# Kernel optimization log

Measured on AMD Instinct MI355X. Metric: run time of the kernel, lower is better.

Reference implementation:

```python
import jax, jax.numpy as jnp
import numpy as np

SPATIAL_DIM = 2
N_IN = 4096
N_OUT = 1024
C_IN = 32
C_OUT = 32
FILTER_SEQ = (64, 64)
BATCH = 16


def _grid(num_points):
    # replicates: meshgrid(indexing='xy') of linspace(0,1,n) per dim, dstack, view(-1, d)
    n = int(num_points ** (1.0 / SPATIAL_DIM))
    nodes = np.linspace(0.0, 1.0, n)
    X, Y = np.meshgrid(nodes, nodes, indexing='xy')
    return np.dstack((X, Y)).reshape(-1, SPATIAL_DIM)  # (n^2, 2)


def _cache():
    # replicates QuadConvLayer.cache(): bump-support sparsity pattern
    out_locs = _grid(N_OUT)               # (N_OUT, 2)
    in_nodes = _grid(N_IN)                # (N_IN, 2)
    locs = out_locs[:, None, :] - in_nodes[None, :, :]   # (N_OUT, N_IN, 2)
    bump_arg = np.linalg.norm(locs, axis=2) ** 4
    decay_param = (N_IN / 16.0) ** 2
    mask = bump_arg <= 1.0 / decay_param
    idx = np.argwhere(mask)               # (E, 2), row-major sorted like torch.nonzero
    eval_locs = locs[mask]                # (E, 2)
    return eval_locs.astype(np.float32), idx.astype(np.int64)


def setup_inputs() -> dict:
    key = jax.random.key(0)
    k_feat, k1, k2, k3 = jax.random.split(key, 4)
    eval_locs, eval_indices = _cache()
    # filter MLP G: Linear(2,64,bias=False) -> Sin -> Linear(64,64) -> Sin -> Linear(64, C_IN*C_OUT)
    d0, d1, d2, d3 = SPATIAL_DIM, FILTER_SEQ[0], FILTER_SEQ[1], C_IN * C_OUT
    W1 = jax.random.normal(k1, (d0, d1), jnp.float32) / np.sqrt(d0)
    W2 = jax.random.normal(k2, (d1, d2), jnp.float32) / np.sqrt(d1)
    W3 = jax.random.normal(k3, (d2, d3), jnp.float32) / np.sqrt(d2)
    features = jax.random.normal(k_feat, (BATCH, C_IN, N_IN), jnp.float32)
    return {
        "features": features,
        "W1": W1,
        "W2": W2,
        "W3": W3,
        "eval_locs": jnp.asarray(eval_locs),
        "eval_indices": jnp.asarray(eval_indices),
    }


def reference(features, W1, W2, W3, eval_locs, eval_indices):
    B = features.shape[0]
    E = eval_locs.shape[0]
    seg = eval_indices[:, 0]   # output point per edge (sorted)
    src = eval_indices[:, 1]   # input point per edge
    # filter MLP with Sin activations: (E, 2) -> (E, C_IN, C_OUT)
    h = jnp.sin(eval_locs @ W1)
    h = jnp.sin(h @ W2)
    filt = (h @ W3).reshape(E, C_IN, C_OUT)
    # gather features at source points: (B, C_IN, E)
    gathered = features[:, :, src]
    # faithful to torch: a raw reshape (NOT a transpose) of (B, C_IN, E) -> (B, E, C_IN)
    g = gathered.reshape(B, E, C_IN)
    vals = jnp.einsum('bni,nij->bnj', g, filt)   # (B, E, C_OUT)
    # faithful raw reshape (B, E, C_OUT) -> (B, C_OUT, E)
    vals = vals.reshape(B, C_OUT, E)
    # scatter-sum over edges into output points (segment_coo sum)
    integral = jnp.zeros((B, C_OUT, N_OUT), features.dtype).at[:, :, seg].add(vals)
    return integral
```

## Files before the change

kernel.cpp:

```cpp
#include <hip/hip_runtime.h>
#include <hip/hip_bf16.h>

typedef __bf16 bf16x4  __attribute__((ext_vector_type(4)));
typedef __bf16 bf16x8  __attribute__((ext_vector_type(8)));
typedef __bf16 bf16x16 __attribute__((ext_vector_type(16)));
typedef float  f32x4   __attribute__((ext_vector_type(4)));

#define N_IN   4096
#define N_OUT  1024
#define BATCH  16
#define ROWS   16

#define H1_STR   72
#define H2_STR   72
#define FT_JSTR  40
#define FTH_NSTR 648
#define G_STR    520
#define V_STR    520
#define GSTR2    1048
#define VSTR2    1288
#define FB_FT_NSTR 1288
#define SEG_STR  34
#define TILE_K   144

#define WS_W3T_OFF    0
#define WS_W2T_OFF    131072
#define WS_FEATT_OFF  139264
#define WS_NEED       4333568

__global__ void qc_zero_kernel(float* __restrict__ out, int n4) {
    int i = blockIdx.x * blockDim.x + threadIdx.x;
    if (i < n4) ((float4*)out)[i] = make_float4(0.f, 0.f, 0.f, 0.f);
}

__global__ void qc_prep_kernel(const float* __restrict__ w3, const float* __restrict__ w2,
                               __bf16* __restrict__ w3t, __bf16* __restrict__ w2t) {
    int gid = blockIdx.x * blockDim.x + threadIdx.x;
    if (gid < 65536) {
        int k = gid & 63, col = gid >> 6;
        w3t[gid] = (__bf16)w3[k * 1024 + col];
    } else {
        int j = gid - 65536;
        int k = j & 63, col = j >> 6;
        w2t[j] = (__bf16)w2[k * 64 + col];
    }
}

__global__ void qc_prep2_kernel(const float* __restrict__ w3, const float* __restrict__ w2,
                                const float* __restrict__ feat,
                                float* __restrict__ out,
                                __bf16* __restrict__ w3t, __bf16* __restrict__ w2t,
                                __bf16* __restrict__ featT) {
    int bid = blockIdx.x, tid = threadIdx.x;
    if (bid < 512) {
        int c    = bid >> 4;
        int src  = (bid & 15) * 256 + tid;
        bf16x16 v;
        #pragma unroll
        for (int b = 0; b < 16; ++b)
            v[b] = (__bf16)feat[(b * 32 + c) * N_IN + src];
        __bf16* p = &featT[((size_t)c * N_IN + src) * 16];
        *(bf16x8*)p       = *(bf16x8*)&v;
        *(bf16x8*)(p + 8) = *((bf16x8*)&v + 1);
    } else if (bid < 528) {
        __shared__ float tile[64][65];
        const int colbase = (bid - 512) * 64;
        #pragma unroll
        for (int it = 0; it < 16; ++it) {
            int k = it * 4 + (tid >> 6);
            int c = tid & 63;
            tile[k][c] = w3[k * 1024 + colbase + c];
        }
        __syncthreads();
        int cc = tid >> 2;
        int k0 = (tid & 3) * 16;
        bf16x8 o0, o1;
        #pragma unroll
        for (int z = 0; z < 8; ++z) {
            o0[z] = (__bf16)tile[k0 + z][cc];
            o1[z] = (__bf16)tile[k0 + 8 + z][cc];
        }
        __bf16* wp = &w3t[(colbase + cc) * 64 + k0];
        *(bf16x8*)wp       = o0;
        *(bf16x8*)(wp + 8) = o1;
    } else if (bid == 528) {
        #pragma unroll
        for (int z = 0; z < 16; ++z) {
            int j = tid * 16 + z;
            w2t[j] = (__bf16)w2[(j & 63) * 64 + (j >> 6)];
        }
    } else {
        int i = (bid - 529) * 256 + tid;
        ((float4*)out)[i] = make_float4(0.f, 0.f, 0.f, 0.f);
    }
}

__global__ __launch_bounds__(512, 2)
void qc_fused32_kernel(const __bf16* __restrict__ featT,
                       const float* __restrict__ w1,
                       const float* __restrict__ locs,
                       const int*   __restrict__ eidx,
                       const __bf16* __restrict__ w2t,
                       const __bf16* __restrict__ w3t,
                       float* __restrict__ out,
                       int E)
{
    __shared__ __align__(16) unsigned char region1[41472];
    __shared__ __align__(16) unsigned char region2[9216];
    __shared__ unsigned short seg_s[32 * SEG_STR];

    __bf16* gb   = (__bf16*)region1;
    __bf16* ftv  = (__bf16*)region1;
    __bf16* vals = (__bf16*)region1;

    __bf16* h1b  = (__bf16*)region2;
    __bf16* h2b  = (__bf16*)(region2 + 9216/2);
    float*  tile = (float*)region2;

    const int tid  = threadIdx.x;
    const int lane = tid & 63;
    const int wv   = tid >> 6;
    const int ml   = lane & 15;
    const int q    = lane >> 4;
    const int n0   = blockIdx.x * 32;
    const int t0   = n0 * 32;
    const int ch0  = t0 / E;
    const int m0   = t0 - ch0 * E;

    const int tlb = wv * 128 + lane;
    bf16x16 gvv[2];
    int sgv[2];
    #pragma unroll
    for (int h = 0; h < 2; ++h) {
        int tl = tlb + h * 64;
        int mm = m0 + tl;
        int cc = ch0 + (mm >= E);
        if (mm >= E) mm -= E;
        int2 p = ((const int2*)eidx)[mm];
        sgv[h] = p.x;
        int ccc = cc < 32 ? cc : 31;
        bf16x16 g = *(const bf16x16*)&featT[((size_t)ccc * N_IN + p.y) * 16];
        if (cc >= 32) {
            #pragma unroll
            for (int z = 0; z < 16; ++z) g[z] = (__bf16)0.f;
        }
        gvv[h] = g;
    }
    const int rg = (wv >> 2) * 16;
    const int cw = (wv & 3) * 16;
    const bf16x8 bw0 = *(const bf16x8*)&w2t[(cw + ml) * 64 + q * 8];
    const bf16x8 bw1 = *(const bf16x8*)&w2t[(cw + ml) * 64 + 32 + q * 8];

    {
        const int r  = tid >> 4;
        const int j0 = (tid & 15) * 4;
        float lx = 0.f, ly = 0.f;
        int n = n0 + r;
        if (n < E) { lx = locs[n * 2]; ly = locs[n * 2 + 1]; }
        float4 wa = *(const float4*)&w1[j0];
        float4 wb = *(const float4*)&w1[64 + j0];
        __bf16* hp = &h1b[r * H1_STR + j0];
        hp[0] = (__bf16)__sinf(lx * wa.x + ly * wb.x);
        hp[1] = (__bf16)__sinf(lx * wa.y + ly * wb.y);
        hp[2] = (__bf16)__sinf(lx * wa.z + ly * wb.z);
        hp[3] = (__bf16)__sinf(lx * wa.w + ly * wb.w);
    }
    __syncthreads();

    {
        bf16x8 a0 = *(const bf16x8*)&h1b[(rg + ml) * H1_STR + q * 8];
        bf16x8 a1 = *(const bf16x8*)&h1b[(rg + ml) * H1_STR + 32 + q * 8];
        f32x4 c = {0.f, 0.f, 0.f, 0.f};
        c = __builtin_amdgcn_mfma_f32_16x16x32_bf16(a0, bw0, c, 0, 0, 0);
        c = __builtin_amdgcn_mfma_f32_16x16x32_bf16(a1, bw1, c, 0, 0, 0);
        #pragma unroll
        for (int g_ = 0; g_ < 4; ++g_)
            h2b[(rg + q * 4 + g_) * H2_STR + cw + ml] = (__bf16)__sinf(c[g_]);
    }

    #pragma unroll
    for (int b = 0; b < 16; ++b) {
        gb[b * GSTR2 + tlb]      = gvv[0][b];
        gb[b * GSTR2 + tlb + 64] = gvv[1][b];
    }
    seg_s[(tlb >> 5) * SEG_STR + (tlb & 31)] = (unsigned short)sgv[0];
    {
        int tl1 = tlb + 64;
        seg_s[(tl1 >> 5) * SEG_STR + (tl1 & 31)] = (unsigned short)sgv[1];
    }
    bf16x8 ag[4];
    #pragma unroll
    for (int rr = 0; rr < 4; ++rr)
        ag[rr] = *(const bf16x8*)&gb[ml * GSTR2 + (wv * 4 + rr) * 32 + q * 8];
    __syncthreads();

    bf16x8 ha00 = *(const bf16x8*)&h2b[ml * H2_STR + q * 8];
    bf16x8 ha01 = *(const bf16x8*)&h2b[ml * H2_STR + 32 + q * 8];
    bf16x8 ha10 = *(const bf16x8*)&h2b[(16 + ml) * H2_STR + q * 8];
    bf16x8 ha11 = *(const bf16x8*)&h2b[(16 + ml) * H2_STR + 32 + q * 8];

    f32x4 c0[4], c1[4];

    {
        f32x4 accA[4], accB[4];
        #pragma unroll
        for (int tt = 0; tt < 4; ++tt) {
            int i_  = wv * 4 + tt;
            int col = i_ * 32 + ml;
            const __bf16* wp = &w3t[col * 64 + q * 8];
            bf16x8 b0 = *(const bf16x8*)wp;
            bf16x8 b1 = *(const bf16x8*)(wp + 32);
            f32x4 cA = {0.f, 0.f, 0.f, 0.f};
            f32x4 cB = {0.f, 0.f, 0.f, 0.f};
            cA = __builtin_amdgcn_mfma_f32_16x16x32_bf16(ha00, b0, cA, 0, 0, 0);
            cA = __builtin_amdgcn_mfma_f32_16x16x32_bf16(ha01, b1, cA, 0, 0, 0);
            cB = __builtin_amdgcn_mfma_f32_16x16x32_bf16(ha10, b0, cB, 0, 0, 0);
            cB = __builtin_amdgcn_mfma_f32_16x16x32_bf16(ha11, b1, cB, 0, 0, 0);
            accA[tt] = cA; accB[tt] = cB;
        }
        #pragma unroll
        for (int g_ = 0; g_ < 4; ++g_) {
            bf16x4 pa, pb;
            #pragma unroll
            for (int tt = 0; tt < 4; ++tt) {
                pa[tt] = (__bf16)accA[tt][g_];
                pb[tt] = (__bf16)accB[tt][g_];
            }
            *(bf16x4*)&ftv[(q * 4 + g_) * FTH_NSTR + ml * FT_JSTR + wv * 4]        = pa;
            *(bf16x4*)&ftv[(16 + q * 4 + g_) * FTH_NSTR + ml * FT_JSTR + wv * 4]   = pb;
        }
    }
    __syncthreads();

    #pragma unroll
    for (int z = 0; z < 5; ++z) {
        int i = tid + z * 512;
        if (i < 16 * TILE_K) tile[i] = 0.f;
    }

    {
        bf16x8 f[4];
        #pragma unroll
        for (int rr = 0; rr < 4; ++rr)
            f[rr] = *(const bf16x8*)&ftv[(wv * 4 + rr) * FTH_NSTR + ml * FT_JSTR + q * 8];
        #pragma unroll
        for (int rr = 0; rr < 4; ++rr) {
            f32x4 z = {0.f, 0.f, 0.f, 0.f};
            c0[rr] = __builtin_amdgcn_mfma_f32_16x16x32_bf16(ag[rr], f[rr], z, 0, 0, 0);
        }
    }
    __syncthreads();

    {
        f32x4 accA[4], accB[4];
        #pragma unroll
        for (int tt = 0; tt < 4; ++tt) {
            int i_  = wv * 4 + tt;
            int col = i_ * 32 + 16 + ml;
            const __bf16* wp = &w3t[col * 64 + q * 8];
            bf16x8 b0 = *(const bf16x8*)wp;
            bf16x8 b1 = *(const bf16x8*)(wp + 32);
            f32x4 cA = {0.f, 0.f, 0.f, 0.f};
            f32x4 cB = {0.f, 0.f, 0.f, 0.f};
            cA = __builtin_amdgcn_mfma_f32_16x16x32_bf16(ha00, b0, cA, 0, 0, 0);
            cA = __builtin_amdgcn_mfma_f32_16x16x32_bf16(ha01, b1, cA, 0, 0, 0);
            cB = __builtin_amdgcn_mfma_f32_16x16x32_bf16(ha10, b0, cB, 0, 0, 0);
            cB = __builtin_amdgcn_mfma_f32_16x16x32_bf16(ha11, b1, cB, 0, 0, 0);
            accA[tt] = cA; accB[tt] = cB;
        }
        #pragma unroll
        for (int g_ = 0; g_ < 4; ++g_) {
            bf16x4 pa, pb;
            #pragma unroll
            for (int tt = 0; tt < 4; ++tt) {
                pa[tt] = (__bf16)accA[tt][g_];
                pb[tt] = (__bf16)accB[tt][g_];
            }
            *(bf16x4*)&ftv[(q * 4 + g_) * FTH_NSTR + ml * FT_JSTR + wv * 4]        = pa;
            *(bf16x4*)&ftv[(16 + q * 4 + g_) * FTH_NSTR + ml * FT_JSTR + wv * 4]   = pb;
        }
    }
    __syncthreads();

    bf16x8 f1[4];
    #pragma unroll
    for (int rr = 0; rr < 4; ++rr)
        f1[rr] = *(const bf16x8*)&ftv[(wv * 4 + rr) * FTH_NSTR + ml * FT_JSTR + q * 8];
    __syncthreads();
    #pragma unroll
    for (int rr = 0; rr < 4; ++rr) {
        f32x4 z = {0.f, 0.f, 0.f, 0.f};
        c1[rr] = __builtin_amdgcn_mfma_f32_16x16x32_bf16(ag[rr], f1[rr], z, 0, 0, 0);
    }
    #pragma unroll
    for (int rr = 0; rr < 4; ++rr) {
        int r = wv * 4 + rr;
        __bf16* vp = &vals[r * FT_JSTR];
        #pragma unroll
        for (int g_ = 0; g_ < 4; ++g_) {
            int b = q * 4 + g_;
            vp[b * VSTR2 + ml]      = (__bf16)c0[rr][g_];
            vp[b * VSTR2 + 16 + ml] = (__bf16)c1[rr][g_];
        }
    }
    __syncthreads();

    {
        const int be = tid >> 5;
        const int w  = tid & 31;
        const __bf16* vp = &vals[be * VSTR2 + w * FT_JSTR];
        bf16x8 v0 = *(const bf16x8*)(vp);
        bf16x8 v1 = *(const bf16x8*)(vp + 8);
        bf16x8 v2 = *(const bf16x8*)(vp + 16);
        bf16x8 v3 = *(const bf16x8*)(vp + 24);
        float vv[32];
        #pragma unroll
        for (int j = 0; j < 8; ++j) {
            vv[j]      = (float)v0[j];
            vv[8 + j]  = (float)v1[j];
            vv[16 + j] = (float)v2[j];
            vv[24 + j] = (float)v3[j];
        }

        const int seg0 = (int)seg_s[0];
        const int segL = (int)seg_s[31 * SEG_STR + 31];
        const int tlw  = E - m0;
        const bool wrap = (tlw < 1024);
        int OFF = 0, NK;
        if (wrap) {
            int tw = tlw - 1;
            OFF = (int)seg_s[(tw >> 5) * SEG_STR + (tw & 31)] - seg0 + 1;
            NK  = OFF + segL + 1;
        } else {
            NK = segL - seg0 + 1;
        }

        int mwin = m0 + (w << 5);
        int cb   = ch0;
        if (mwin >= E) { mwin -= E; ++cb; }
        int jcross = E - mwin;

        if (NK <= TILE_K) {
            const int NEG = -0x40000000;
            int io0 = (cb < 32) ? ((cb == ch0) ? -seg0 : OFF) : NEG;
            int io1 = (cb + 1 < 32) ? OFF : NEG;
            int key_prev = -1;
            float acc = 0.f;
            #pragma unroll
            for (int j = 0; j < 32; ++j) {
                int io = (j < jcross) ? io0 : io1;
                if (io != NEG) {
                    int key = io + (int)seg_s[w * SEG_STR + j];
                    if (key != key_prev) {
                        if (key_prev >= 0) atomicAdd(&tile[be * TILE_K + key_prev], acc);
                        key_prev = key;
                        acc = vv[j];
                    } else {
                        acc += vv[j];
                    }
                }
            }
            if (key_prev >= 0) atomicAdd(&tile[be * TILE_K + key_prev], acc);

            __syncthreads();

            for (int bb = 0; bb < 16; ++bb) {
                for (int i = tid; i < NK; i += 512) {
                    int cbx, sg;
                    if (wrap && i >= OFF) { cbx = ch0 + 1; sg = i - OFF; }
                    else                  { cbx = ch0;     sg = seg0 + i; }
                    if (cbx < 32) {
                        float v = tile[bb * TILE_K + i];
                        int o = (bb << 15) | (cbx << 10) | sg;
                        bool bnd = (i == 0) || (i == NK - 1) ||
                                   (wrap && (i == OFF - 1 || i == OFF));
                        if (bnd) atomicAdd(&out[o], v);
                        else     out[o] = v;
                    }
                }
            }
        } else {
            int base0 = (cb < 32)     ? ((be << 15) | (cb << 10))       : -1;
            int base1 = (cb + 1 < 32) ? ((be << 15) | ((cb + 1) << 10)) : -1;
            int key_prev = -1;
            float acc = 0.f;
            #pragma unroll
            for (int j = 0; j < 32; ++j) {
                int basej = (j < jcross) ? base0 : base1;
                if (basej >= 0) {
                    int key = basej + (int)seg_s[w * SEG_STR + j];
                    if (key != key_prev) {
                        if (key_prev >= 0) atomicAdd(&out[key_prev], acc);
                        key_prev = key;
                        acc = vv[j];
                    } else {
                        acc += vv[j];
                    }
                }
            }
            if (key_prev >= 0) atomicAdd(&out[key_prev], acc);
        }
    }
}

__global__ __launch_bounds__(256, 2)
void qc_main_kernel(const float* __restrict__ feat,
                    const float* __restrict__ w1,
                    const float* __restrict__ w2,
                    const float* __restrict__ locs,
                    const int*   __restrict__ eidx,
                    const __bf16* __restrict__ w3t,
                    float* __restrict__ out,
                    int E)
{
    __shared__ __align__(16) __bf16 h1b[ROWS * H1_STR];
    __shared__ __align__(16) __bf16 h2b[ROWS * H2_STR];
    __shared__ __align__(16) __bf16 ftv[ROWS * FB_FT_NSTR];
    __shared__ __align__(16) __bf16 gb [BATCH * G_STR];
    __shared__ unsigned short seg_s[512];
    __shared__ unsigned short src_s[512];

    const int tid = threadIdx.x;
    const int n0  = blockIdx.x * ROWS;
    const int t0  = n0 * 32;
    const int ch0 = t0 / E;
    const int m0  = t0 - ch0 * E;

    {
        const int r  = tid >> 4;
        const int j0 = (tid & 15) * 4;
        float lx = 0.f, ly = 0.f;
        int n = n0 + r;
        if (n < E) { lx = locs[n * 2]; ly = locs[n * 2 + 1]; }
        float4 wa = *(const float4*)&w1[j0];
        float4 wb = *(const float4*)&w1[64 + j0];
        __bf16* h = &h1b[r * H1_STR + j0];
        h[0] = (__bf16)__sinf(lx * wa.x + ly * wb.x);
        h[1] = (__bf16)__sinf(lx * wa.y + ly * wb.y);
        h[2] = (__bf16)__sinf(lx * wa.z + ly * wb.z);
        h[3] = (__bf16)__sinf(lx * wa.w + ly * wb.w);
    }
    for (int tl = tid; tl < 512; tl += 256) {
        int mm = m0 + tl; if (mm >= E) mm -= E;
        seg_s[tl] = (unsigned short)eidx[mm * 2];
        src_s[tl] = (unsigned short)eidx[mm * 2 + 1];
    }
    __syncthreads();

    {
        const int r  = tid >> 4;
        const int j0 = (tid & 15) * 4;
        float a0 = 0.f, a1 = 0.f, a2 = 0.f, a3 = 0.f;
        const __bf16* h1r = &h1b[r * H1_STR];
        #pragma unroll 8
        for (int k = 0; k < 64; ++k) {
            float h = (float)h1r[k];
            float4 w = *(const float4*)&w2[k * 64 + j0];
            a0 += h * w.x; a1 += h * w.y; a2 += h * w.z; a3 += h * w.w;
        }
        __bf16* h = &h2b[r * H2_STR + j0];
        h[0] = (__bf16)__sinf(a0);
        h[1] = (__bf16)__sinf(a1);
        h[2] = (__bf16)__sinf(a2);
        h[3] = (__bf16)__sinf(a3);
    }
    #pragma unroll 4
    for (int it = 0; it < 32; ++it) {
        int idx = it * 256 + tid;
        int b   = idx >> 9;
        int tl  = idx & 511;
        int mm  = m0 + tl;
        int cc  = ch0 + (mm >= E);
        if (mm >= E) mm -= E;
        float v = 0.f;
        if (cc < 32) v = feat[(b * 32 + cc) * N_IN + (int)src_s[tl]];
        gb[b * G_STR + tl] = (__bf16)v;
    }
    __syncthreads();

    const int lane = tid & 63;
    const int wv   = tid >> 6;
    const int ml   = lane & 15;
    const int q    = lane >> 4;

    {
        bf16x8 a0 = *(const bf16x8*)&h2b[ml * H2_STR + q * 8];
        bf16x8 a1 = *(const bf16x8*)&h2b[ml * H2_STR + 32 + q * 8];
        #pragma unroll
        for (int t = 0; t < 16; ++t) {
            int col = wv * 256 + t * 16 + ml;
            const __bf16* wp = &w3t[col * 64 + q * 8];
            bf16x8 b0 = *(const bf16x8*)wp;
            bf16x8 b1 = *(const bf16x8*)(wp + 32);
            f32x4 c = {0.f, 0.f, 0.f, 0.f};
            c = __builtin_amdgcn_mfma_f32_16x16x32_bf16(a0, b0, c, 0, 0, 0);
            c = __builtin_amdgcn_mfma_f32_16x16x32_bf16(a1, b1, c, 0, 0, 0);
            int i_ = col >> 5, j_ = col & 31;
            __bf16* fp = &ftv[j_ * FT_JSTR + i_];
            fp[(q * 4 + 0) * FB_FT_NSTR] = (__bf16)c[0];
            fp[(q * 4 + 1) * FB_FT_NSTR] = (__bf16)c[1];
            fp[(q * 4 + 2) * FB_FT_NSTR] = (__bf16)c[2];
            fp[(q * 4 + 3) * FB_FT_NSTR] = (__bf16)c[3];
        }
    }
    __syncthreads();

    {
        bf16x8 ag[4], f0[4], f1[4];
        #pragma unroll
        for (int rr = 0; rr < 4; ++rr) {
            int r = wv * 4 + rr;
            ag[rr] = *(const bf16x8*)&gb[ml * G_STR + r * 32 + q * 8];
            f0[rr] = *(const bf16x8*)&ftv[r * FB_FT_NSTR + ml        * FT_JSTR + q * 8];
            f1[rr] = *(const bf16x8*)&ftv[r * FB_FT_NSTR + (16 + ml) * FT_JSTR + q * 8];
        }
        __syncthreads();
        __bf16* valsb = ftv;
        #pragma unroll
        for (int rr = 0; rr < 4; ++rr) {
            int r = wv * 4 + rr;
            f32x4 c0 = {0.f, 0.f, 0.f, 0.f};
            f32x4 c1 = {0.f, 0.f, 0.f, 0.f};
            c0 = __builtin_amdgcn_mfma_f32_16x16x32_bf16(ag[rr], f0[rr], c0, 0, 0, 0);
            c1 = __builtin_amdgcn_mfma_f32_16x16x32_bf16(ag[rr], f1[rr], c1, 0, 0, 0);
            __bf16* vp = &valsb[r * 32];
            #pragma unroll
            for (int g_ = 0; g_ < 4; ++g_) {
                int b = q * 4 + g_;
                vp[b * V_STR + ml]      = (__bf16)c0[g_];
                vp[b * V_STR + 16 + ml] = (__bf16)c1[g_];
            }
        }
    }
    __syncthreads();

    {
        const __bf16* valsb = ftv;
        const int b = tid >> 4;
        const int r = tid & 15;
        const __bf16* vp = &valsb[b * V_STR + r * 32];
        bf16x8 v0 = *(const bf16x8*)(vp);
        bf16x8 v1 = *(const bf16x8*)(vp + 8);
        bf16x8 v2 = *(const bf16x8*)(vp + 16);
        bf16x8 v3 = *(const bf16x8*)(vp + 24);
        float vv[32];
        #pragma unroll
        for (int j = 0; j < 8; ++j) {
            vv[j]      = (float)v0[j];
            vv[8 + j]  = (float)v1[j];
            vv[16 + j] = (float)v2[j];
            vv[24 + j] = (float)v3[j];
        }
        const int tl0 = r * 32;
        int key_prev = -1;
        float acc = 0.f;
        #pragma unroll
        for (int j = 0; j < 32; ++j) {
            int mm = m0 + tl0 + j;
            int cc = ch0 + (mm >= E);
            if (mm >= E) mm -= E;
            if (cc < 32) {
                int o   = (int)seg_s[tl0 + j];
                int key = ((b * 32 + cc) << 10) | o;
                if (key != key_prev) {
                    if (key_prev >= 0) atomicAdd(&out[key_prev], acc);
                    key_prev = key;
                    acc = vv[j];
                } else {
                    acc += vv[j];
                }
            }
        }
        if (key_prev >= 0) atomicAdd(&out[key_prev], acc);
    }
}

extern "C" void kernel_launch(void* const* d_in, const int* in_sizes, int n_in,
                              void* d_out, int out_size, void* d_ws, size_t ws_size,
                              hipStream_t stream)
{
    (void)n_in;
    const float* feat = (const float*)d_in[0];
    const float* w1   = (const float*)d_in[1];
    const float* w2   = (const float*)d_in[2];
    const float* w3   = (const float*)d_in[3];
    const float* locs = (const float*)d_in[4];
    const int*   eidx = (const int*)d_in[5];
    float* out  = (float*)d_out;

    const int E = in_sizes[4] / 2;
    if (E <= 0) return;

    __bf16* w3t   = (__bf16*)((char*)d_ws + WS_W3T_OFF);
    __bf16* w2t   = (__bf16*)((char*)d_ws + WS_W2T_OFF);
    __bf16* featT = (__bf16*)((char*)d_ws + WS_FEATT_OFF);

    if (ws_size >= (size_t)WS_NEED) {
        int nblocks = (E + 31) / 32;
        qc_prep2_kernel<<<1041, 256, 0, stream>>>(w3, w2, feat, out, w3t, w2t, featT);
        qc_fused32_kernel<<<nblocks, 512, 0, stream>>>(featT, w1, locs, eidx, w2t, w3t, out, E);
    } else {
        int n4 = out_size / 4;
        int nblocks = (E + ROWS - 1) / ROWS;
        qc_zero_kernel<<<(n4 + 255) / 256, 256, 0, stream>>>(out, n4);
        qc_prep_kernel<<<272, 256, 0, stream>>>(w3, w2, w3t, w2t);
        qc_main_kernel<<<nblocks, 256, 0, stream>>>(feat, w1, w2, locs, eidx, w3t, out, E);
    }
}
```

Before: 127.3 us.

## Use per-wave vals slabs to drop block barriers and flatten tile flush loop

Each wave now writes its MFMA results into a private LDS slab and reads them back itself, so two block-wide __syncthreads around the vals exchange are removed. Lane-to-work mapping changes so each lane handles one batch row of its own wave's data. The final tile flush becomes a single flattened loop over NK*16 elements instead of a batch loop with a mostly idle inner loop, and TILE_K shrinks. The risk is a different LDS bank-conflict pattern and a possible overrun of the tile buffer, since TILE_K is now smaller.

```diff
diff --git a/kernel.cpp b/kernel.cpp
--- a/kernel.cpp
+++ b/kernel.cpp
@@ -18,10 +18,10 @@
 #define G_STR    520
 #define V_STR    520
 #define GSTR2    1048
-#define VSTR2    1288
 #define FB_FT_NSTR 1288
 #define SEG_STR  34
-#define TILE_K   144
+#define WSLAB    2592
+#define TILE_K   132
 
 #define WS_W3T_OFF    0
 #define WS_W2T_OFF    131072
@@ -282,33 +282,45 @@
     }
     __syncthreads();
 
-    bf16x8 f1[4];
-    #pragma unroll
-    for (int rr = 0; rr < 4; ++rr)
-        f1[rr] = *(const bf16x8*)&ftv[(wv * 4 + rr) * FTH_NSTR + ml * FT_JSTR + q * 8];
-    __syncthreads();
-    #pragma unroll
-    for (int rr = 0; rr < 4; ++rr) {
-        f32x4 z = {0.f, 0.f, 0.f, 0.f};
-        c1[rr] = __builtin_amdgcn_mfma_f32_16x16x32_bf16(ag[rr], f1[rr], z, 0, 0, 0);
-    }
-    #pragma unroll
-    for (int rr = 0; rr < 4; ++rr) {
-        int r = wv * 4 + rr;
-        __bf16* vp = &vals[r * FT_JSTR];
-        #pragma unroll
-        for (int g_ = 0; g_ < 4; ++g_) {
-            int b = q * 4 + g_;
-            vp[b * VSTR2 + ml]      = (__bf16)c0[rr][g_];
-            vp[b * VSTR2 + 16 + ml] = (__bf16)c1[rr][g_];
-        }
-    }
-    __syncthreads();
-
-    {
-        const int be = tid >> 5;
-        const int w  = tid & 31;
-        const __bf16* vp = &vals[be * VSTR2 + w * FT_JSTR];
+    const int seg0 = (int)seg_s[0];
+    const int segL = (int)seg_s[31 * SEG_STR + 31];
+    const int tlw  = E - m0;
+    const bool wrap = (tlw < 1024);
+    int OFF = 0, NK;
+    if (wrap) {
+        int tw = tlw - 1;
+        OFF = (int)seg_s[(tw >> 5) * SEG_STR + (tw & 31)] - seg0 + 1;
+        NK  = OFF + segL + 1;
+    } else {
+        NK = segL - seg0 + 1;
+    }
+
+    {
+        bf16x8 f1[4];
+        #pragma unroll
+        for (int rr = 0; rr < 4; ++rr)
+            f1[rr] = *(const bf16x8*)&ftv[(wv * 4 + rr) * FTH_NSTR + ml * FT_JSTR + q * 8];
+        #pragma unroll
+        for (int rr = 0; rr < 4; ++rr) {
+            f32x4 z = {0.f, 0.f, 0.f, 0.f};
+            c1[rr] = __builtin_amdgcn_mfma_f32_16x16x32_bf16(ag[rr], f1[rr], z, 0, 0, 0);
+        }
+        __bf16* vslab = &vals[wv * WSLAB];
+        #pragma unroll
+        for (int rr = 0; rr < 4; ++rr) {
+            __bf16* vp = &vslab[rr * FTH_NSTR];
+            #pragma unroll
+            for (int g_ = 0; g_ < 4; ++g_) {
+                int b = q * 4 + g_;
+                vp[b * FT_JSTR + ml]      = (__bf16)c0[rr][g_];
+                vp[b * FT_JSTR + 16 + ml] = (__bf16)c1[rr][g_];
+            }
+        }
+
+        const int q2 = lane >> 4;
+        const int b  = lane & 15;
+        const int w  = wv * 4 + q2;
+        const __bf16* vp = &vslab[q2 * FTH_NSTR + b * FT_JSTR];
         bf16x8 v0 = *(const bf16x8*)(vp);
         bf16x8 v1 = *(const bf16x8*)(vp + 8);
         bf16x8 v2 = *(const bf16x8*)(vp + 16);
@@ -320,19 +332,6 @@
             vv[8 + j]  = (float)v1[j];
             vv[16 + j] = (float)v2[j];
             vv[24 + j] = (float)v3[j];
-        }
-
-        const int seg0 = (int)seg_s[0];
-        const int segL = (int)seg_s[31 * SEG_STR + 31];
-        const int tlw  = E - m0;
-        const bool wrap = (tlw < 1024);
-        int OFF = 0, NK;
-        if (wrap) {
-            int tw = tlw - 1;
-            OFF = (int)seg_s[(tw >> 5) * SEG_STR + (tw & 31)] - seg0 + 1;
-            NK  = OFF + segL + 1;
-        } else {
-            NK = segL - seg0 + 1;
         }
 
         int mwin = m0 + (w << 5);
@@ -352,7 +351,7 @@
                 if (io != NEG) {
                     int key = io + (int)seg_s[w * SEG_STR + j];
                     if (key != key_prev) {
-                        if (key_prev >= 0) atomicAdd(&tile[be * TILE_K + key_prev], acc);
+                        if (key_prev >= 0) atomicAdd(&tile[b * TILE_K + key_prev], acc);
                         key_prev = key;
                         acc = vv[j];
                     } else {
@@ -360,28 +359,10 @@
                     }
                 }
             }
-            if (key_prev >= 0) atomicAdd(&tile[be * TILE_K + key_prev], acc);
-
-            __syncthreads();
-
-            for (int bb = 0; bb < 16; ++bb) {
-                for (int i = tid; i < NK; i += 512) {
-                    int cbx, sg;
-                    if (wrap && i >= OFF) { cbx = ch0 + 1; sg = i - OFF; }
-                    else                  { cbx = ch0;     sg = seg0 + i; }
-                    if (cbx < 32) {
-                        float v = tile[bb * TILE_K + i];
-                        int o = (bb << 15) | (cbx << 10) | sg;
-                        bool bnd = (i == 0) || (i == NK - 1) ||
-                                   (wrap && (i == OFF - 1 || i == OFF));
-                        if (bnd) atomicAdd(&out[o], v);
-                        else     out[o] = v;
-                    }
-                }
-            }
+            if (key_prev >= 0) atomicAdd(&tile[b * TILE_K + key_prev], acc);
         } else {
-            int base0 = (cb < 32)     ? ((be << 15) | (cb << 10))       : -1;
-            int base1 = (cb + 1 < 32) ? ((be << 15) | ((cb + 1) << 10)) : -1;
+            int base0 = (cb < 32)     ? ((b << 15) | (cb << 10))       : -1;
+            int base1 = (cb + 1 < 32) ? ((b << 15) | ((cb + 1) << 10)) : -1;
             int key_prev = -1;
             float acc = 0.f;
             #pragma unroll
@@ -399,6 +380,27 @@
                 }
             }
             if (key_prev >= 0) atomicAdd(&out[key_prev], acc);
+        }
+    }
+
+    if (NK <= TILE_K) {
+        __syncthreads();
+
+        int total = NK * 16;
+        for (int t = tid; t < total; t += 512) {
+            int bb = t / NK;
+            int i  = t - bb * NK;
+            int cbx, sg;
+            if (wrap && i >= OFF) { cbx = ch0 + 1; sg = i - OFF; }
+            else                  { cbx = ch0;     sg = seg0 + i; }
+            if (cbx < 32) {
+                float v = tile[bb * TILE_K + i];
+                int o = (bb << 15) | (cbx << 10) | sg;
+                bool bnd = (i == 0) || (i == NK - 1) ||
+                           (wrap && (i == OFF - 1 || i == OFF));
+                if (bnd) atomicAdd(&out[o], v);
+                else     out[o] = v;
+            }
         }
     }
 }
```

Result: faster. 121.9 us (median of 3 runs) (-4.2%).
